# Kernel optimization log

Measured on AMD Instinct MI355X. Metric: run time of the kernel, lower is better.

## Reference

```python
import math
import jax, jax.numpy as jnp
import numpy as np

KSIZE = (5, 5)
SIGMA = (1.0, 1.0)
LOW_T = 0.1
HIGH_T = 0.2
EPS = 1e-6

# Sobel first-order kernels (cross-correlation form, unnormalized as in canny)
SOBEL = np.array([[[-1., 0., 1.], [-2., 0., 2.], [-1., 0., 1.]],
                  [[-1., -2., -1.], [0., 0., 0.], [1., 2., 1.]]], np.float32)

# Neighbor offsets in kornia's direction order: 0deg=right, going clockwise
_OFFS = [(1, 2), (2, 2), (2, 1), (2, 0), (1, 0), (0, 0), (0, 1), (0, 2)]

def _nms_kernels():
    k = np.zeros((8, 1, 3, 3), np.float32)
    k[:, 0, 1, 1] = 1.0
    for i, (r, c) in enumerate(_OFFS):
        k[i, 0, r, c] = -1.0
    return jnp.asarray(k)

def _hysteresis_kernels():
    k = np.zeros((8, 1, 3, 3), np.float32)
    for i, (r, c) in enumerate(_OFFS):
        k[i, 0, r, c] = 1.0
    return jnp.asarray(k)

def _gaussian_kernel1d(ksize, sigma):
    x = jnp.arange(ksize, dtype=jnp.float32) - ksize // 2
    if ksize % 2 == 0:
        x = x + 0.5
    g = jnp.exp(-x * x / (2.0 * sigma * sigma))
    return g / g.sum()

def _conv_depthwise_same(x, k2d, pad_mode):
    # x: [B, C, H, W]; k2d: [kh, kw]; cross-correlation with 'same' output
    b, c, h, w = x.shape
    kh, kw = k2d.shape
    xp = jnp.pad(x, ((0, 0), (0, 0),
                     ((kh - 1) // 2, kh - 1 - (kh - 1) // 2),
                     ((kw - 1) // 2, kw - 1 - (kw - 1) // 2)), mode=pad_mode)
    xr = xp.reshape(b * c, 1, h + kh - 1, w + kw - 1)
    out = jax.lax.conv_general_dilated(xr, k2d[None, None].astype(x.dtype), (1, 1), 'VALID')
    return out.reshape(b, c, h, w)

def _conv_multi(x, w, p):
    # x: [B, 1, H, W], w: [O, 1, kh, kw], zero padding p
    return jax.lax.conv_general_dilated(x, w.astype(x.dtype), (1, 1), [(p, p), (p, p)])

def canny_fwd(x):
    dtype = x.dtype
    if x.shape[1] == 3:  # rgb -> grayscale
        wgt = jnp.array([0.299, 0.587, 0.114], dtype)
        x = jnp.einsum('bchw,c->bhw', x, wgt)[:, None]
    # Gaussian blur, separable, reflect padding
    kx = _gaussian_kernel1d(KSIZE[1], SIGMA[1])
    ky = _gaussian_kernel1d(KSIZE[0], SIGMA[0])
    blurred = _conv_depthwise_same(x, kx[None, :], 'reflect')
    blurred = _conv_depthwise_same(blurred, ky[:, None], 'reflect')
    # Sobel gradients, replicate padding, unnormalized
    gx = _conv_depthwise_same(blurred, jnp.asarray(SOBEL[0]), 'edge')
    gy = _conv_depthwise_same(blurred, jnp.asarray(SOBEL[1]), 'edge')
    magnitude = jnp.sqrt(gx * gx + gy * gy + EPS)  # [B,1,H,W]
    # quantized gradient direction index in {0..7}
    ang = jnp.round(jnp.arctan2(gy, gx) * (180.0 / math.pi) / 45.0)
    # direction-aware non-maximum suppression
    nms_mag = _conv_multi(magnitude, _nms_kernels(), 1)  # [B,8,H,W]
    pos = jnp.mod(ang, 8.0).astype(jnp.int32)
    neg = jnp.mod(ang + 4.0, 8.0).astype(jnp.int32)
    sel_p = jnp.take_along_axis(nms_mag, pos, axis=1)
    sel_n = jnp.take_along_axis(nms_mag, neg, axis=1)
    is_max = jnp.minimum(sel_p, sel_n) > 0.0
    magnitude = magnitude * is_max
    # double threshold: weak=0.5, strong=1.0
    low = (magnitude > LOW_T).astype(dtype)
    high = (magnitude > HIGH_T).astype(dtype)
    edges = (low + high) * 0.5
    # hysteresis: grow strong into weak until fixed point (flood fill)
    hk = _hysteresis_kernels()
    edges0 = jax.lax.stop_gradient(edges)

    def body(carry):
        e, _ = carry
        weak = (e == 0.5).astype(dtype)
        strong = (e == 1.0).astype(dtype)
        nb = _conv_multi(e, hk, 1)  # 8 neighbor values
        mag = jnp.any(nb == 1.0, axis=1, keepdims=True).astype(dtype)
        mag = mag * weak + strong
        return mag + (mag == 0.0) * weak * 0.5, e

    def cond(carry):
        e, e_old = carry
        return jnp.any(e != e_old)

    e_final, _ = jax.lax.while_loop(cond, body, (edges0, -jnp.ones_like(edges0)))
    # at the fixed point the returned hysteresis magnitude is exactly (edges == 1)
    edges_out = (e_final == 1.0).astype(dtype)
    return magnitude, edges_out

def setup_inputs() -> dict:
    key = jax.random.key(0)
    x = jax.random.uniform(key, (4, 3, 1024, 1024), dtype=jnp.float32)
    return {'x': x}

def reference(x):
    return canny_fwd(x)
```

## Files before the change

### kernel.cpp

```cpp
#include <hip/hip_runtime.h>
#include <math.h>

static constexpr int BB  = 4;
static constexpr int HH  = 1024;
static constexpr int WW  = 1024;
static constexpr int HWP = HH * WW;
static constexpr int NPIX = BB * HWP;
static constexpr int WPR = WW / 64;
static constexpr int PW  = HWP / 64;
static constexpr int ROUNDS = 6;
static constexpr int NT  = BB * 8 * 8;
static constexpr int RF  = ROUNDS + 1;
static constexpr int FCN = RF + RF * NT;

static constexpr int TX = 64, TY = 8;
static constexpr int GH = 16,  GW = 72;
static constexpr int HBH = 16, HBW = 68;
static constexpr int VBH = 12, VBW = 68;
static constexpr int MGH = 10, MGW = 66;

__device__ __forceinline__ int reflect_idx(int i, int n) {
    i = (i < 0) ? -i : i;
    return (i >= n) ? (2 * n - 2 - i) : i;
}

__global__ void __launch_bounds__(256) k_front(const float* __restrict__ x,
                                               float* __restrict__ out0,
                                               unsigned long long* __restrict__ weakP,
                                               unsigned long long* __restrict__ strongP,
                                               int* __restrict__ fc,
                                               double w0, double w1, double w2) {
    __shared__ double A[GH * GW];
    __shared__ double B[HBH * HBW];
    __shared__ unsigned char P[TY * TX];

    const int tid = threadIdx.x;
    const int x0  = blockIdx.x * TX;
    const int y0  = blockIdx.y * TY;
    const int b   = blockIdx.z;
    const float* base = x + (size_t)b * 3u * HWP;

    if (blockIdx.x == 0 && blockIdx.y == 0 && b == 0) {
        for (int i = tid; i < FCN; i += 256)
            fc[i] = (i == 0 || (i >= RF && i < RF + NT)) ? 1 : 0;
    }

    for (int idx = tid; idx < GH * GW; idx += 256) {
        int r = idx / GW, c = idx - r * GW;
        int gyr = reflect_idx(y0 + r - 4, HH);
        int gxr = reflect_idx(x0 + c - 4, WW);
        const float* rp = base + (size_t)gyr * WW;
        double rr = (double)rp[gxr];
        double gg = (double)rp[HWP + gxr];
        double bb = (double)rp[2 * HWP + gxr];
        A[idx] = rr * 0.299 + gg * 0.587 + bb * 0.114;
    }
    __syncthreads();

    for (int idx = tid; idx < HBH * HBW; idx += 256) {
        int r = idx / HBW, c = idx - r * HBW;
        const double* g = &A[r * GW + c];
        double s;
        s  = w0 * g[0];
        s += w1 * g[1];
        s += w2 * g[2];
        s += w1 * g[3];
        s += w0 * g[4];
        B[idx] = s;
    }
    __syncthreads();

    for (int idx = tid; idx < VBH * VBW; idx += 256) {
        int r = idx / VBW, c = idx - r * VBW;
        const double* h = &B[r * HBW + c];
        double s;
        s  = w0 * h[0];
        s += w1 * h[1 * HBW];
        s += w2 * h[2 * HBW];
        s += w1 * h[3 * HBW];
        s += w0 * h[4 * HBW];
        A[idx] = s;
    }
    __syncthreads();

    for (int idx = tid; idx < MGH * MGW; idx += 256) {
        int r = idx / MGW, c = idx - r * MGW;
        int gy = y0 + r - 1, gx = x0 + c - 1;
        double mg2 = 0.0;
        if (gy >= 0 && gy < HH && gx >= 0 && gx < WW) {
            int ym = gy > 0 ? gy - 1 : 0, yp = gy < HH - 1 ? gy + 1 : HH - 1;
            int xm = gx > 0 ? gx - 1 : 0, xp = gx < WW - 1 ? gx + 1 : WW - 1;
            auto BL = [&](int yy, int xx) -> double {
                return A[(yy - y0 + 2) * VBW + (xx - x0 + 2)];
            };
            double b00 = BL(ym, xm), b01 = BL(ym, gx), b02 = BL(ym, xp);
            double b10 = BL(gy, xm),                   b12 = BL(gy, xp);
            double b20 = BL(yp, xm), b21 = BL(yp, gx), b22 = BL(yp, xp);
            double gxv = -b00 + b02 - 2.0 * b10 + 2.0 * b12 - b20 + b22;
            double gyv = -b00 - 2.0 * b01 - b02 + b20 + 2.0 * b21 + b22;
            mg2 = gxv * gxv + gyv * gyv + 1e-6;
            if (r >= 1 && r < TY + 1 && c >= 1 && c < TX + 1) {
                double ax = fabs(gxv), ay = fabs(gyv);
                int p;
                if (ay < 0.41421356237309503 * ax)
                    p = (gxv >= 0.0) ? 0 : 4;
                else if (ay < 2.4142135623730951 * ax)
                    p = (gyv >= 0.0) ? ((gxv >= 0.0) ? 1 : 3)
                                     : ((gxv >= 0.0) ? 7 : 5);
                else
                    p = (gyv >= 0.0) ? 2 : 6;
                P[(r - 1) * TX + (c - 1)] = (unsigned char)p;
            }
        }
        B[r * MGW + c] = mg2;
    }
    __syncthreads();

    for (int k = 0; k < (TX * TY) / 256; ++k) {
        int idx = k * 256 + tid;
        int r = idx >> 6, c = idx & 63;
        double ctr2 = B[(r + 1) * MGW + (c + 1)];
        int p = P[idx];
        int dr = ((425   >> (2 * p)) & 3) - 1;
        int dc = ((36890 >> (2 * p)) & 3) - 1;
        double mp2 = B[(r + 1 + dr) * MGW + (c + 1 + dc)];
        double mn2 = B[(r + 1 - dr) * MGW + (c + 1 - dc)];
        bool ismax = (ctr2 > mp2) && (ctr2 > mn2);
        out0[(size_t)b * HWP + (size_t)(y0 + r) * WW + (x0 + c)] =
            ismax ? (float)sqrt(ctr2) : 0.0f;
        bool strong = ismax && (ctr2 > 0.04);
        bool weak   = ismax && (ctr2 > 0.01) && !strong;
        unsigned long long wb = __ballot(weak);
        unsigned long long sb = __ballot(strong);
        if ((tid & 63) == 0) {
            int word = (y0 + r) * WPR + (x0 >> 6);
            weakP[(size_t)b * PW + word]   = wb;
            strongP[(size_t)b * PW + word] = sb;
        }
    }
}

__device__ __forceinline__ unsigned long long ks_fill(unsigned long long g, unsigned long long p) {
    unsigned long long q;
    q = p;        g |= q & (g << 1);
    q &= q << 1;  g |= q & (g << 2);
    q &= q << 2;  g |= q & (g << 4);
    q &= q << 4;  g |= q & (g << 8);
    q &= q << 8;  g |= q & (g << 16);
    q &= q << 16; g |= q & (g << 32);
    q = p;        g |= q & (g >> 1);
    q &= q >> 1;  g |= q & (g >> 2);
    q &= q >> 2;  g |= q & (g >> 4);
    q &= q >> 4;  g |= q & (g >> 8);
    q &= q >> 8;  g |= q & (g >> 16);
    q &= q >> 16; g |= q & (g >> 32);
    return g;
}

__global__ void __launch_bounds__(256) k_pass(const unsigned long long* __restrict__ weakP,
                                              unsigned long long* __restrict__ strongP,
                                              int* __restrict__ flags,
                                              int* __restrict__ dirt,
                                              float* __restrict__ out1, int rr) {
    __shared__ unsigned long long S[128][2];
    __shared__ int chf[4];

    const int tid  = threadIdx.x;
    const int lane = tid & 63;
    const int w    = tid >> 6;
    const int wy   = w >> 1, wx = w & 1;
    const int tile = blockIdx.x;
    const int b  = tile >> 6;
    const int ty = (tile >> 3) & 7;
    const int tx = tile & 7;
    const int tb = b << 6;

    unsigned long long* spl = strongP + (size_t)b * PW;
    const int row  = (ty << 7) + (wy << 6) + lane;
    const int wc   = (tx << 1) + wx;
    const int wi   = row * WPR + wc;
    const int lrow = (wy << 6) + lane;

    const bool active = (flags[rr - 1] != 0);
    if (!active && rr != ROUNDS) return;

    int go = 0;
    if (active) {
        const int* d0 = dirt + (size_t)(rr - 1) * NT;
        if (ty > 0) { go |= d0[tb + ((ty - 1) << 3) + tx];
                      if (tx > 0) go |= d0[tb + ((ty - 1) << 3) + tx - 1];
                      if (tx < 7) go |= d0[tb + ((ty - 1) << 3) + tx + 1]; }
        if (ty < 7) { go |= d0[tb + ((ty + 1) << 3) + tx];
                      if (tx > 0) go |= d0[tb + ((ty + 1) << 3) + tx - 1];
                      if (tx < 7) go |= d0[tb + ((ty + 1) << 3) + tx + 1]; }
        if (tx > 0) go |= d0[tb + (ty << 3) + tx - 1];
        if (tx < 7) go |= d0[tb + (ty << 3) + tx + 1];
    }

    if (go) {
        const unsigned long long* wp = weakP + (size_t)b * PW;
        unsigned long long wv = wp[wi];
        unsigned long long s  = spl[wi];

        unsigned long long ho_ext = 0;
        if (wx == 0) { if (tx > 0) ho_ext = spl[wi - 1] >> 63; }
        else         { if (tx < 7) ho_ext = spl[wi + 1] << 63; }
        unsigned long long topE = 0, botE = 0;
        unsigned long long topC = 0, botC = 0;
        if (lane == 0) {
            if (wy == 0) {
                if (ty > 0) {
                    int ra = row - 1;
                    unsigned long long hs = spl[ra * WPR + wc];
                    topE = (hs << 1) | hs | (hs >> 1);
                    if (wc > 0)  topE |= spl[ra * WPR + wc - 1] >> 63;
                    if (wc < 15) topE |= spl[ra * WPR + wc + 1] << 63;
                }
            } else {
                int rb = row - 1;
                if (wx == 0) { if (tx > 0) topC = spl[rb * WPR + wc - 1] >> 63; }
                else         { if (tx < 7) topC = spl[rb * WPR + wc + 1] << 63; }
            }
        }
        if (lane == 63) {
            if (wy == 1) {
                if (ty < 7) {
                    int ra = row + 1;
                    unsigned long long hs = spl[ra * WPR + wc];
                    botE = (hs << 1) | hs | (hs >> 1);
                    if (wc > 0)  botE |= spl[ra * WPR + wc - 1] >> 63;
                    if (wc < 15) botE |= spl[ra * WPR + wc + 1] << 63;
                }
            } else {
                int rb = row + 1;
                if (wx == 0) { if (tx > 0) botC = spl[rb * WPR + wc - 1] >> 63; }
                else         { if (tx < 7) botC = spl[rb * WPR + wc + 1] << 63; }
            }
        }

        S[lrow][wx] = s;
        if (lane == 0) chf[w] = 0;
        __syncthreads();

        unsigned long long pub = s;
        int blkchanged = 0;
        for (;;) {
            unsigned long long partner = S[lrow][wx ^ 1];
            unsigned long long ho = ho_ext | ((wx == 1) ? (partner >> 63) : (partner << 63));
            unsigned long long top = 0, bot = 0;
            if (lane == 0) {
                if (wy == 1) {
                    unsigned long long a = S[63][wx], p2 = S[63][wx ^ 1];
                    top = (a << 1) | a | (a >> 1) |
                          ((wx == 1) ? (p2 >> 63) : (p2 << 63)) | topC;
                } else top = topE;
            }
            if (lane == 63) {
                if (wy == 0) {
                    unsigned long long a = S[64][wx], p2 = S[64][wx ^ 1];
                    bot = (a << 1) | a | (a >> 1) |
                          ((wx == 1) ? (p2 >> 63) : (p2 << 63)) | botC;
                } else bot = botE;
            }

            for (;;) {
                unsigned long long sp = (s << 1) | s | (s >> 1) | ho;
                unsigned long long up = __shfl_up(sp, 1);
                unsigned long long dn = __shfl_down(sp, 1);
                if (lane == 0)  up = top;
                if (lane == 63) dn = bot;
                unsigned long long g = s | (wv & (up | sp | dn));
                g = ks_fill(g, wv);
                int ch = (g != s);
                s = g;
                if (!__any(ch)) break;
            }

            int wch = __any(s != pub);
            if (lane == 0) chf[w] = wch;
            __syncthreads();
            S[lrow][wx] = s;
            pub = s;
            int any = chf[0] | chf[1] | chf[2] | chf[3];
            if (any) blkchanged = 1;
            __syncthreads();
            if (!any) break;
        }

        if (blkchanged) {
            spl[wi] = s;
            if (tid == 0) {
                dirt[(size_t)rr * NT + tb + (ty << 3) + tx] = 1;
                atomicOr(&flags[rr], 1);
            }
        }
    }

    if (rr == ROUNDS) {
        if (!go) S[lrow][wx] = spl[wi];
        __syncthreads();
        float* o = out1 + (size_t)b * HWP;
        for (int it = 0; it < 16; ++it) {
            int fi = (it << 8) + tid;
            int r  = fi >> 5;
            int c4 = fi & 31;
            unsigned long long bits = S[r][c4 >> 4];
            int sh = (c4 & 15) << 2;
            float4 v;
            v.x = ((bits >> (sh + 0)) & 1ull) ? 1.0f : 0.0f;
            v.y = ((bits >> (sh + 1)) & 1ull) ? 1.0f : 0.0f;
            v.z = ((bits >> (sh + 2)) & 1ull) ? 1.0f : 0.0f;
            v.w = ((bits >> (sh + 3)) & 1ull) ? 1.0f : 0.0f;
            int grow = (ty << 7) + r;
            int gcol = (tx << 7) + (c4 << 2);
            *reinterpret_cast<float4*>(&o[(size_t)grow * WW + gcol]) = v;
        }
    }
}

extern "C" void kernel_launch(void* const* d_in, const int* in_sizes, int n_in,
                              void* d_out, int out_size, void* d_ws, size_t ws_size,
                              hipStream_t stream) {
    const float* x = (const float*)d_in[0];
    float* out0 = (float*)d_out;
    float* out1 = out0 + NPIX;

    unsigned long long* weakP   = (unsigned long long*)d_ws;
    unsigned long long* strongP = weakP + (size_t)BB * PW;
    int* fc    = (int*)(strongP + (size_t)BB * PW);
    int* flags = fc;
    int* dirt  = fc + RF;

    double g0 = exp(-2.0), g1 = exp(-0.5), g2 = 1.0;
    double sum = (((g0 + g1) + g2) + g1) + g0;
    double w0 = g0 / sum, w1 = g1 / sum, w2 = g2 / sum;

    k_front<<<dim3(WW / TX, HH / TY, BB), dim3(256), 0, stream>>>(
        x, out0, weakP, strongP, fc, w0, w1, w2);

    for (int r = 1; r <= ROUNDS; ++r)
        k_pass<<<dim3(NT), dim3(256), 0, stream>>>(weakP, strongP, flags, dirt, out1, r);
}
```

Before: 142.3 us.

## Enlarge hysteresis tiles to 256x256 with four bit-words per lane

The hysteresis pass now uses 4x4 tiles per image of 256x256 pixels instead of 8x8 tiles of 128x128. Each lane keeps four 64-bit words of a row in registers, so horizontal carry is handled inside the lane. Waves are stacked vertically and exchange only their boundary rows through shared memory. This aims to cut inter-block boundary propagation and round count, at the cost of fewer blocks (64) and less parallelism per pass. The launch code (not shown) presumably has to change its grid size to match.

```diff
diff --git a/kernel.cpp b/kernel.cpp
--- a/kernel.cpp
+++ b/kernel.cpp
@@ -9,7 +9,7 @@
 static constexpr int WPR = WW / 64;
 static constexpr int PW  = HWP / 64;
 static constexpr int ROUNDS = 6;
-static constexpr int NT  = BB * 8 * 8;
+static constexpr int NT  = BB * 4 * 4;
 static constexpr int RF  = ROUNDS + 1;
 static constexpr int FCN = RF + RF * NT;
 
@@ -162,24 +162,18 @@
                                               int* __restrict__ flags,
                                               int* __restrict__ dirt,
                                               float* __restrict__ out1, int rr) {
-    __shared__ unsigned long long S[128][2];
+    __shared__ unsigned long long S[256][4];
+    __shared__ unsigned long long Btop[4][4], Bbot[4][4];
     __shared__ int chf[4];
 
     const int tid  = threadIdx.x;
     const int lane = tid & 63;
     const int w    = tid >> 6;
-    const int wy   = w >> 1, wx = w & 1;
     const int tile = blockIdx.x;
-    const int b  = tile >> 6;
-    const int ty = (tile >> 3) & 7;
-    const int tx = tile & 7;
-    const int tb = b << 6;
-
-    unsigned long long* spl = strongP + (size_t)b * PW;
-    const int row  = (ty << 7) + (wy << 6) + lane;
-    const int wc   = (tx << 1) + wx;
-    const int wi   = row * WPR + wc;
-    const int lrow = (wy << 6) + lane;
+    const int b  = tile >> 4;
+    const int ty = (tile >> 2) & 3;
+    const int tx = tile & 3;
+    const int tb = b << 4;
 
     const bool active = (flags[rr - 1] != 0);
     if (!active && rr != ROUNDS) return;
@@ -187,100 +181,113 @@
     int go = 0;
     if (active) {
         const int* d0 = dirt + (size_t)(rr - 1) * NT;
-        if (ty > 0) { go |= d0[tb + ((ty - 1) << 3) + tx];
-                      if (tx > 0) go |= d0[tb + ((ty - 1) << 3) + tx - 1];
-                      if (tx < 7) go |= d0[tb + ((ty - 1) << 3) + tx + 1]; }
-        if (ty < 7) { go |= d0[tb + ((ty + 1) << 3) + tx];
-                      if (tx > 0) go |= d0[tb + ((ty + 1) << 3) + tx - 1];
-                      if (tx < 7) go |= d0[tb + ((ty + 1) << 3) + tx + 1]; }
-        if (tx > 0) go |= d0[tb + (ty << 3) + tx - 1];
-        if (tx < 7) go |= d0[tb + (ty << 3) + tx + 1];
-    }
+        for (int dy = -1; dy <= 1; ++dy) {
+            int yy = ty + dy;
+            if (yy < 0 || yy > 3) continue;
+            for (int dx = -1; dx <= 1; ++dx) {
+                int xx = tx + dx;
+                if (xx < 0 || xx > 3 || (dy == 0 && dx == 0)) continue;
+                go |= d0[tb + (yy << 2) + xx];
+            }
+        }
+    }
+
+    unsigned long long* spl      = strongP + (size_t)b * PW;
+    const unsigned long long* wp = weakP + (size_t)b * PW;
+    const int lr   = (w << 6) + lane;
+    const int row  = (ty << 8) + lr;
+    const int wc0  = tx << 2;
+    const int base = row * WPR + wc0;
+
+    unsigned long long s0, s1, s2, s3;
 
     if (go) {
-        const unsigned long long* wp = weakP + (size_t)b * PW;
-        unsigned long long wv = wp[wi];
-        unsigned long long s  = spl[wi];
-
-        unsigned long long ho_ext = 0;
-        if (wx == 0) { if (tx > 0) ho_ext = spl[wi - 1] >> 63; }
-        else         { if (tx < 7) ho_ext = spl[wi + 1] << 63; }
-        unsigned long long topE = 0, botE = 0;
-        unsigned long long topC = 0, botC = 0;
-        if (lane == 0) {
-            if (wy == 0) {
-                if (ty > 0) {
-                    int ra = row - 1;
-                    unsigned long long hs = spl[ra * WPR + wc];
-                    topE = (hs << 1) | hs | (hs >> 1);
-                    if (wc > 0)  topE |= spl[ra * WPR + wc - 1] >> 63;
-                    if (wc < 15) topE |= spl[ra * WPR + wc + 1] << 63;
-                }
-            } else {
-                int rb = row - 1;
-                if (wx == 0) { if (tx > 0) topC = spl[rb * WPR + wc - 1] >> 63; }
-                else         { if (tx < 7) topC = spl[rb * WPR + wc + 1] << 63; }
-            }
-        }
-        if (lane == 63) {
-            if (wy == 1) {
-                if (ty < 7) {
-                    int ra = row + 1;
-                    unsigned long long hs = spl[ra * WPR + wc];
-                    botE = (hs << 1) | hs | (hs >> 1);
-                    if (wc > 0)  botE |= spl[ra * WPR + wc - 1] >> 63;
-                    if (wc < 15) botE |= spl[ra * WPR + wc + 1] << 63;
-                }
-            } else {
-                int rb = row + 1;
-                if (wx == 0) { if (tx > 0) botC = spl[rb * WPR + wc - 1] >> 63; }
-                else         { if (tx < 7) botC = spl[rb * WPR + wc + 1] << 63; }
-            }
-        }
-
-        S[lrow][wx] = s;
-        if (lane == 0) chf[w] = 0;
+        unsigned long long wv0 = wp[base + 0], wv1 = wp[base + 1];
+        unsigned long long wv2 = wp[base + 2], wv3 = wp[base + 3];
+        s0 = spl[base + 0]; s1 = spl[base + 1];
+        s2 = spl[base + 2]; s3 = spl[base + 3];
+
+        unsigned long long hoL = 0, hoR = 0;
+        if (tx > 0) hoL = spl[base - 1] >> 63;
+        if (tx < 3) hoR = spl[base + 4] << 63;
+
+        unsigned long long topE[4] = {0, 0, 0, 0}, botE[4] = {0, 0, 0, 0};
+        if (w == 0 && lane == 0 && ty > 0) {
+            int ra = (row - 1) * WPR;
+            unsigned long long h[6];
+            for (int k = 0; k < 6; ++k) {
+                int wq = wc0 + k - 1;
+                h[k] = (wq >= 0 && wq < WPR) ? spl[ra + wq] : 0ull;
+            }
+            for (int j = 0; j < 4; ++j)
+                topE[j] = (h[j+1] << 1) | h[j+1] | (h[j+1] >> 1) | (h[j] >> 63) | (h[j+2] << 63);
+        }
+        if (w == 3 && lane == 63 && ty < 3) {
+            int ra = (row + 1) * WPR;
+            unsigned long long h[6];
+            for (int k = 0; k < 6; ++k) {
+                int wq = wc0 + k - 1;
+                h[k] = (wq >= 0 && wq < WPR) ? spl[ra + wq] : 0ull;
+            }
+            for (int j = 0; j < 4; ++j)
+                botE[j] = (h[j+1] << 1) | h[j+1] | (h[j+1] >> 1) | (h[j] >> 63) | (h[j+2] << 63);
+        }
+
+        if (lane == 0 || lane == 63) {
+            unsigned long long o0 = (s0 << 1) | s0 | (s0 >> 1) | hoL | (s1 << 63);
+            unsigned long long o1 = (s1 << 1) | s1 | (s1 >> 1) | (s0 >> 63) | (s2 << 63);
+            unsigned long long o2 = (s2 << 1) | s2 | (s2 >> 1) | (s1 >> 63) | (s3 << 63);
+            unsigned long long o3 = (s3 << 1) | s3 | (s3 >> 1) | (s2 >> 63) | hoR;
+            if (lane == 0)  { Btop[w][0] = o0; Btop[w][1] = o1; Btop[w][2] = o2; Btop[w][3] = o3; }
+            else            { Bbot[w][0] = o0; Bbot[w][1] = o1; Bbot[w][2] = o2; Bbot[w][3] = o3; }
+        }
         __syncthreads();
 
-        unsigned long long pub = s;
         int blkchanged = 0;
         for (;;) {
-            unsigned long long partner = S[lrow][wx ^ 1];
-            unsigned long long ho = ho_ext | ((wx == 1) ? (partner >> 63) : (partner << 63));
-            unsigned long long top = 0, bot = 0;
+            unsigned long long up0 = 0, up1 = 0, up2 = 0, up3 = 0;
+            unsigned long long dn0 = 0, dn1 = 0, dn2 = 0, dn3 = 0;
             if (lane == 0) {
-                if (wy == 1) {
-                    unsigned long long a = S[63][wx], p2 = S[63][wx ^ 1];
-                    top = (a << 1) | a | (a >> 1) |
-                          ((wx == 1) ? (p2 >> 63) : (p2 << 63)) | topC;
-                } else top = topE;
+                if (w > 0) { up0 = Bbot[w-1][0]; up1 = Bbot[w-1][1]; up2 = Bbot[w-1][2]; up3 = Bbot[w-1][3]; }
+                else       { up0 = topE[0]; up1 = topE[1]; up2 = topE[2]; up3 = topE[3]; }
             }
             if (lane == 63) {
-                if (wy == 0) {
-                    unsigned long long a = S[64][wx], p2 = S[64][wx ^ 1];
-                    bot = (a << 1) | a | (a >> 1) |
-                          ((wx == 1) ? (p2 >> 63) : (p2 << 63)) | botC;
-                } else bot = botE;
-            }
-
+                if (w < 3) { dn0 = Btop[w+1][0]; dn1 = Btop[w+1][1]; dn2 = Btop[w+1][2]; dn3 = Btop[w+1][3]; }
+                else       { dn0 = botE[0]; dn1 = botE[1]; dn2 = botE[2]; dn3 = botE[3]; }
+            }
+
+            int innerch = 0;
             for (;;) {
-                unsigned long long sp = (s << 1) | s | (s >> 1) | ho;
-                unsigned long long up = __shfl_up(sp, 1);
-                unsigned long long dn = __shfl_down(sp, 1);
-                if (lane == 0)  up = top;
-                if (lane == 63) dn = bot;
-                unsigned long long g = s | (wv & (up | sp | dn));
-                g = ks_fill(g, wv);
-                int ch = (g != s);
-                s = g;
+                unsigned long long sp0 = (s0 << 1) | s0 | (s0 >> 1) | hoL | (s1 << 63);
+                unsigned long long sp1 = (s1 << 1) | s1 | (s1 >> 1) | (s0 >> 63) | (s2 << 63);
+                unsigned long long sp2 = (s2 << 1) | s2 | (s2 >> 1) | (s1 >> 63) | (s3 << 63);
+                unsigned long long sp3 = (s3 << 1) | s3 | (s3 >> 1) | (s2 >> 63) | hoR;
+                unsigned long long u0 = __shfl_up(sp0, 1), d0 = __shfl_down(sp0, 1);
+                unsigned long long u1 = __shfl_up(sp1, 1), d1 = __shfl_down(sp1, 1);
+                unsigned long long u2 = __shfl_up(sp2, 1), d2 = __shfl_down(sp2, 1);
+                unsigned long long u3 = __shfl_up(sp3, 1), d3 = __shfl_down(sp3, 1);
+                if (lane == 0)  { u0 = up0; u1 = up1; u2 = up2; u3 = up3; }
+                if (lane == 63) { d0 = dn0; d1 = dn1; d2 = dn2; d3 = dn3; }
+                unsigned long long g0 = ks_fill(s0 | (wv0 & (u0 | sp0 | d0)), wv0);
+                unsigned long long g1 = ks_fill(s1 | (wv1 & (u1 | sp1 | d1)), wv1);
+                unsigned long long g2 = ks_fill(s2 | (wv2 & (u2 | sp2 | d2)), wv2);
+                unsigned long long g3 = ks_fill(s3 | (wv3 & (u3 | sp3 | d3)), wv3);
+                int ch = (g0 != s0) | (g1 != s1) | (g2 != s2) | (g3 != s3);
+                s0 = g0; s1 = g1; s2 = g2; s3 = g3;
                 if (!__any(ch)) break;
-            }
-
-            int wch = __any(s != pub);
-            if (lane == 0) chf[w] = wch;
+                innerch = 1;
+            }
+
+            if (lane == 0) chf[w] = innerch;
             __syncthreads();
-            S[lrow][wx] = s;
-            pub = s;
+            if (lane == 0 || lane == 63) {
+                unsigned long long o0 = (s0 << 1) | s0 | (s0 >> 1) | hoL | (s1 << 63);
+                unsigned long long o1 = (s1 << 1) | s1 | (s1 >> 1) | (s0 >> 63) | (s2 << 63);
+                unsigned long long o2 = (s2 << 1) | s2 | (s2 >> 1) | (s1 >> 63) | (s3 << 63);
+                unsigned long long o3 = (s3 << 1) | s3 | (s3 >> 1) | (s2 >> 63) | hoR;
+                if (lane == 0)  { Btop[w][0] = o0; Btop[w][1] = o1; Btop[w][2] = o2; Btop[w][3] = o3; }
+                else            { Bbot[w][0] = o0; Bbot[w][1] = o1; Bbot[w][2] = o2; Bbot[w][3] = o3; }
+            }
             int any = chf[0] | chf[1] | chf[2] | chf[3];
             if (any) blkchanged = 1;
             __syncthreads();
@@ -288,22 +295,25 @@
         }
 
         if (blkchanged) {
-            spl[wi] = s;
+            spl[base + 0] = s0; spl[base + 1] = s1;
+            spl[base + 2] = s2; spl[base + 3] = s3;
             if (tid == 0) {
-                dirt[(size_t)rr * NT + tb + (ty << 3) + tx] = 1;
+                dirt[(size_t)rr * NT + tb + (ty << 2) + tx] = 1;
                 atomicOr(&flags[rr], 1);
             }
         }
     }
 
     if (rr == ROUNDS) {
-        if (!go) S[lrow][wx] = spl[wi];
+        if (go) { S[lr][0] = s0; S[lr][1] = s1; S[lr][2] = s2; S[lr][3] = s3; }
+        else    { S[lr][0] = spl[base + 0]; S[lr][1] = spl[base + 1];
+                  S[lr][2] = spl[base + 2]; S[lr][3] = spl[base + 3]; }
         __syncthreads();
         float* o = out1 + (size_t)b * HWP;
-        for (int it = 0; it < 16; ++it) {
+        for (int it = 0; it < 64; ++it) {
             int fi = (it << 8) + tid;
-            int r  = fi >> 5;
-            int c4 = fi & 31;
+            int r  = fi >> 6;
+            int c4 = fi & 63;
             unsigned long long bits = S[r][c4 >> 4];
             int sh = (c4 & 15) << 2;
             float4 v;
@@ -311,8 +321,8 @@
             v.y = ((bits >> (sh + 1)) & 1ull) ? 1.0f : 0.0f;
             v.z = ((bits >> (sh + 2)) & 1ull) ? 1.0f : 0.0f;
             v.w = ((bits >> (sh + 3)) & 1ull) ? 1.0f : 0.0f;
-            int grow = (ty << 7) + r;
-            int gcol = (tx << 7) + (c4 << 2);
+            int grow = (ty << 8) + r;
+            int gcol = (tx << 8) + (c4 << 2);
             *reinterpret_cast<float4*>(&o[(size_t)grow * WW + gcol]) = v;
         }
     }
```

Result: slower. 159.6 us (+12.1%).
